# Performance work log

Hardware: AMD Instinct MI355X
Metric: run time of the kernel (lower is better)

Reference implementation:

```python
import jax, jax.numpy as jnp
import numpy as np

DIM = 512
HEADS = 8
DIM_HEAD = 64
INNER = HEADS * DIM_HEAD  # 512
EPS = 1e-5


def _per_head_layernorm(t, gamma, beta):
    # t: [b, h, n, k]; gamma/beta: [h, k] (distinct LayerNorm per head)
    mu = jnp.mean(t, axis=-1, keepdims=True)
    var = jnp.mean(jnp.square(t - mu), axis=-1, keepdims=True)
    t_hat = (t - mu) * jax.lax.rsqrt(var + EPS)
    return t_hat * gamma[None, :, None, :] + beta[None, :, None, :]


def setup_inputs() -> dict:
    key = jax.random.key(0)
    ks = jax.random.split(key, 6)
    x = jax.random.normal(ks[0], (4, 8192, DIM), dtype=jnp.float32)
    # xavier_normal_ with gain=1e-4 on to_qkv weight [3*inner, dim]
    std_qkv = 1e-4 * np.sqrt(2.0 / (3 * INNER + DIM))
    W_qkv = jax.random.normal(ks[1], (3 * INNER, DIM), dtype=jnp.float32) * std_qkv
    gamma_K = jnp.ones((HEADS, DIM_HEAD), dtype=jnp.float32)
    beta_K = jnp.zeros((HEADS, DIM_HEAD), dtype=jnp.float32)
    gamma_V = jnp.ones((HEADS, DIM_HEAD), dtype=jnp.float32)
    beta_V = jnp.zeros((HEADS, DIM_HEAD), dtype=jnp.float32)
    std_out = np.sqrt(1.0 / INNER)
    W_out = jax.random.uniform(ks[2], (DIM, INNER), dtype=jnp.float32, minval=-std_out, maxval=std_out)
    b_out = jax.random.uniform(ks[3], (DIM,), dtype=jnp.float32, minval=-std_out, maxval=std_out)
    return {"x": x, "W_qkv": W_qkv, "gamma_K": gamma_K, "beta_K": beta_K,
            "gamma_V": gamma_V, "beta_V": beta_V, "W_out": W_out, "b_out": b_out}


def reference(x, W_qkv, gamma_K, beta_K, gamma_V, beta_V, W_out, b_out):
    b, n, _ = x.shape
    qkv = jnp.einsum('bnd,ed->bne', x, W_qkv)  # [b, n, 3*inner]
    q, k, v = jnp.split(qkv, 3, axis=-1)

    def to_heads(t):  # [b, n, h*k] -> [b, h, n, k]
        return t.reshape(b, n, HEADS, DIM_HEAD).transpose(0, 2, 1, 3)

    q, k, v = to_heads(q), to_heads(k), to_heads(v)
    k = _per_head_layernorm(k, gamma_K, beta_K)
    v = _per_head_layernorm(v, gamma_V, beta_V)

    # Galerkin linear attention: (K^T V)/n then Q @ (.)  -> O(n * d^2)
    p_attn = jnp.einsum('bhnk,bhnv->bhkv', k, v) / n  # [b, h, k, k]
    out = jnp.einsum('bhnk,bhkv->bhnv', q, p_attn)    # [b, h, n, k]
    out = out.transpose(0, 2, 1, 3).reshape(b, n, INNER)
    return jnp.einsum('bne,de->bnd', out, W_out) + b_out
```

## Files before the change

### kernel.cpp

```cpp
#include <hip/hip_runtime.h>


typedef __attribute__((ext_vector_type(8))) short bf16x8;
typedef __attribute__((ext_vector_type(4))) float f32x4;
typedef __attribute__((ext_vector_type(4))) unsigned short u16x4;
typedef __attribute__((ext_vector_type(4))) unsigned int u32x4;

__device__ __forceinline__ unsigned short f2bf(float f) {
  unsigned int u = __builtin_bit_cast(unsigned int, f);
  u += 0x7FFFu + ((u >> 16) & 1u);
  return (unsigned short)(u >> 16);
}

__device__ __forceinline__ float bf2f(unsigned short h) {
  unsigned int u = ((unsigned int)h) << 16;
  return __builtin_bit_cast(float, u);
}

__device__ __forceinline__ unsigned int cvt2(float lo, float hi) {
  return ((unsigned int)f2bf(hi) << 16) | (unsigned int)f2bf(lo);
}

__device__ __forceinline__ f32x4 mfma16(bf16x8 a, bf16x8 b, f32x4 c) {
  return __builtin_amdgcn_mfma_f32_16x16x32_bf16(a, b, c, 0, 0, 0);
}

__device__ __forceinline__ void gload16(const void* g, void* l) {
  __builtin_amdgcn_global_load_lds(
      (const __attribute__((address_space(1))) void*)g,
      (__attribute__((address_space(3))) void*)l, 16, 0, 0);
}

__global__ void k_cvt_w(const float* __restrict__ Wqkv,
                        const float* __restrict__ Wout,
                        unsigned short* __restrict__ Wb,
                        unsigned short* __restrict__ Wob) {
  int i = blockIdx.x * 256 + threadIdx.x;
  const float4* src;
  u16x4* dst;
  if (i < 196608) { src = (const float4*)Wqkv + i; dst = (u16x4*)Wb + i; }
  else { i -= 196608; src = (const float4*)Wout + i; dst = (u16x4*)Wob + i; }
  float4 v = *src;
  u16x4 o;
  o[0] = f2bf(v.x); o[1] = f2bf(v.y); o[2] = f2bf(v.z); o[3] = f2bf(v.w);
  *dst = o;
}

__launch_bounds__(256, 3)
__global__ void k1_kvp(const float* __restrict__ x,
                       const unsigned short* __restrict__ wqkvb,
                       const float* __restrict__ gK, const float* __restrict__ bK,
                       const float* __restrict__ gV, const float* __restrict__ bV,
                       unsigned short* __restrict__ Ppart) {
  __shared__ __align__(16) unsigned short As[8192];
  __shared__ __align__(16) unsigned short Bs[8192];
  const int bid = (int)blockIdx.x;
  const int wgid = (bid & 7) * 256 + (bid >> 3);
  const int rt = wgid >> 3, h = wgid & 7;
  const int tid = (int)threadIdx.x;
  const int l = tid & 63, w = tid >> 6;
  const int wr = w >> 1, wc = w & 1;
  const int g = l >> 4, c16 = l & 15;
  const int row0 = rt * 128;
  const int swz = ((l & 7) ^ (l >> 3)) * 8;

  const float* gx = x + (size_t)(row0 + w * 32 + (l >> 3)) * 512 + swz;
  const int bcol = (w < 2) ? (512 + h * 64 + w * 32) : (1024 + h * 64 + (w - 2) * 32);
  const unsigned short* gsB = wqkvb + (bcol + (l >> 3)) * 512 + swz;
  unsigned short* la = As + w * 2048 + l * 8;

  f32x4 acc[4][4] = {};
  float4 pf[8];

#pragma unroll
  for (int j = 0; j < 4; ++j) {
    pf[2 * j]     = *(const float4*)(gx + j * 4096);
    pf[2 * j + 1] = *(const float4*)(gx + j * 4096 + 4);
  }

  for (int kt = 0; kt < 8; ++kt) {
#pragma unroll
    for (int j = 0; j < 4; ++j) {
      u32x4 c;
      c[0] = cvt2(pf[2 * j].x, pf[2 * j].y);
      c[1] = cvt2(pf[2 * j].z, pf[2 * j].w);
      c[2] = cvt2(pf[2 * j + 1].x, pf[2 * j + 1].y);
      c[3] = cvt2(pf[2 * j + 1].z, pf[2 * j + 1].w);
      *(u32x4*)(la + j * 512) = c;
    }
#pragma unroll
    for (int j = 0; j < 4; ++j)
      gload16(gsB + kt * 64 + j * 8 * 512, Bs + w * 2048 + j * 512);
    __builtin_amdgcn_sched_barrier(0);
    if (kt < 7) {
#pragma unroll
      for (int j = 0; j < 4; ++j) {
        pf[2 * j]     = *(const float4*)(gx + (kt + 1) * 64 + j * 4096);
        pf[2 * j + 1] = *(const float4*)(gx + (kt + 1) * 64 + j * 4096 + 4);
      }
      asm volatile("s_waitcnt vmcnt(8) lgkmcnt(0)" ::: "memory");
    } else {
      asm volatile("s_waitcnt vmcnt(0) lgkmcnt(0)" ::: "memory");
    }
    __builtin_amdgcn_sched_barrier(0);
    __builtin_amdgcn_s_barrier();
#pragma unroll
    for (int ks = 0; ks < 2; ++ks) {
      const int kcol = (ks * 32 + g * 8) ^ ((c16 & 7) << 3);
      bf16x8 af[4], bfv[4];
#pragma unroll
      for (int mi = 0; mi < 4; ++mi)
        af[mi] = *(const bf16x8*)&As[(wr * 64 + mi * 16 + c16) * 64 + kcol];
#pragma unroll
      for (int ni = 0; ni < 4; ++ni)
        bfv[ni] = *(const bf16x8*)&Bs[(wc * 64 + ni * 16 + c16) * 64 + kcol];
#pragma unroll
      for (int mi = 0; mi < 4; ++mi)
#pragma unroll
        for (int ni = 0; ni < 4; ++ni)
          acc[mi][ni] = mfma16(af[mi], bfv[ni], acc[mi][ni]);
    }
    __builtin_amdgcn_sched_barrier(0);
    __builtin_amdgcn_s_barrier();
  }

  const float* gamma = (wc == 0) ? gK : gV;
  const float* beta  = (wc == 0) ? bK : bV;
  float gm[4], bt[4];
#pragma unroll
  for (int ni = 0; ni < 4; ++ni) {
    gm[ni] = gamma[h * 64 + ni * 16 + c16];
    bt[ni] = beta[h * 64 + ni * 16 + c16];
  }
  unsigned short* dst = (wc == 0) ? As : Bs;
#pragma unroll
  for (int mi = 0; mi < 4; ++mi) {
    float mean4[4], rs4[4];
#pragma unroll
    for (int r = 0; r < 4; ++r) {
      float a0 = acc[mi][0][r], a1 = acc[mi][1][r];
      float a2 = acc[mi][2][r], a3 = acc[mi][3][r];
      float s1 = a0 + a1 + a2 + a3;
      float s2 = a0 * a0 + a1 * a1 + a2 * a2 + a3 * a3;
#pragma unroll
      for (int m = 1; m <= 8; m <<= 1) {
        s1 += __shfl_xor(s1, m, 64);
        s2 += __shfl_xor(s2, m, 64);
      }
      const float mean = s1 * (1.0f / 64.0f);
      const float var = s2 * (1.0f / 64.0f) - mean * mean;
      mean4[r] = mean;
      rs4[r] = rsqrtf(var + 1e-5f);
    }
    const int n0 = wr * 64 + mi * 16 + g * 4;
#pragma unroll
    for (int ni = 0; ni < 4; ++ni) {
      u16x4 o;
#pragma unroll
      for (int r = 0; r < 4; ++r)
        o[r] = f2bf((acc[mi][ni][r] - mean4[r]) * rs4[r] * gm[ni] + bt[ni]);
      *(u16x4*)&dst[(ni * 16 + c16) * 128 + (((n0 >> 3) ^ c16) << 3) + (n0 & 7)] = o;
    }
  }
  __syncthreads();

  f32x4 pacc[4] = {};
#pragma unroll
  for (int ks = 0; ks < 4; ++ks) {
    const int grp = ((ks * 4 + g) ^ c16) << 3;
    bf16x8 af = *(const bf16x8*)&As[(w * 16 + c16) * 128 + grp];
#pragma unroll
    for (int ni = 0; ni < 4; ++ni) {
      bf16x8 bv = *(const bf16x8*)&Bs[(ni * 16 + c16) * 128 + grp];
      pacc[ni] = mfma16(af, bv, pacc[ni]);
    }
  }
  const int bh = (rt >> 6) * 8 + h;
  unsigned short* Pp = Ppart + ((size_t)(bh * 64 + (rt & 63))) * 4096;
#pragma unroll
  for (int ni = 0; ni < 4; ++ni)
#pragma unroll
    for (int r = 0; r < 4; ++r)
      Pp[(w * 16 + g * 4 + r) * 64 + ni * 16 + c16] = f2bf(pacc[ni][r]);
}

__launch_bounds__(256)
__global__ void k_preduce(const unsigned short* __restrict__ Ppart,
                          float* __restrict__ P) {
  const int bh = blockIdx.x;
  const int e = blockIdx.y * 256 + threadIdx.x;
  const unsigned short* src = Ppart + (size_t)bh * 64 * 4096 + e;
  float s = 0.f;
#pragma unroll 8
  for (int sl = 0; sl < 64; ++sl) s += bf2f(src[sl * 4096]);
  P[bh * 4096 + e] = s;
}

__launch_bounds__(256)
__global__ void k3a_g(const float* __restrict__ Wqkv,
                      const float* __restrict__ P,
                      unsigned short* __restrict__ Gt) {
  __shared__ float Pl[64 * 64];
  const int bh = blockIdx.x, dd = blockIdx.y;
  const int b = bh >> 3, h = bh & 7;
  const int t = (int)threadIdx.x;
  for (int i = t; i < 1024; i += 256)
    ((float4*)Pl)[i] = ((const float4*)(P + bh * 4096))[i];
  __syncthreads();

  const int qg = t >> 6, dl = t & 63;
  const int d = dd * 64 + dl;
  float acc[16] = {};
  for (int dh = 0; dh < 64; ++dh) {
    const float wq = Wqkv[(h * 64 + dh) * 512 + d];
    const float* pr = &Pl[dh * 64 + qg * 16];
#pragma unroll
    for (int i = 0; i < 16; ++i) acc[i] += pr[i] * wq;
  }
  unsigned short* go = &Gt[(b * 512 + d) * 512 + h * 64 + qg * 16];
#pragma unroll
  for (int i = 0; i < 16; ++i) go[i] = f2bf(acc[i] * (1.0f / 8192.0f));
}

__device__ __forceinline__ void stage_tile(const unsigned short* pa,
                                           const unsigned short* pb,
                                           unsigned short* As, unsigned short* Bs,
                                           int w) {
#pragma unroll
  for (int j = 0; j < 4; ++j) {
    gload16(pa + j * 8 * 512, As + w * 2048 + j * 512);
    gload16(pb + j * 8 * 512, Bs + w * 2048 + j * 512);
  }
}

__device__ __forceinline__ void compute_tile(const unsigned short* As,
                                             const unsigned short* Bs,
                                             int wr, int wc, int g, int c16,
                                             f32x4 acc[4][4]) {
#pragma unroll
  for (int ks = 0; ks < 2; ++ks) {
    const int kcol = (ks * 32 + g * 8) ^ ((c16 & 7) << 3);
    bf16x8 af[4], bfv[4];
#pragma unroll
    for (int mi = 0; mi < 4; ++mi)
      af[mi] = *(const bf16x8*)&As[(wr * 64 + mi * 16 + c16) * 64 + kcol];
#pragma unroll
    for (int ni = 0; ni < 4; ++ni)
      bfv[ni] = *(const bf16x8*)&Bs[(wc * 64 + ni * 16 + c16) * 64 + kcol];
#pragma unroll
    for (int mi = 0; mi < 4; ++mi)
#pragma unroll
      for (int ni = 0; ni < 4; ++ni)
        acc[mi][ni] = mfma16(af[mi], bfv[ni], acc[mi][ni]);
  }
}

__launch_bounds__(256)
__global__ void k3b_m(const unsigned short* __restrict__ wob,
                      const unsigned short* __restrict__ Gt,
                      unsigned short* __restrict__ Mb) {
  __shared__ __align__(16) unsigned short As[8192];
  __shared__ __align__(16) unsigned short Bs[8192];
  const int rt = blockIdx.x, ct = blockIdx.y, b = blockIdx.z;
  const int tid = (int)threadIdx.x;
  const int l = tid & 63, w = tid >> 6;
  const int wr = w >> 1, wc = w & 1;
  const int g = l >> 4, c16 = l & 15;
  const int row0 = rt * 128, col0 = ct * 128;
  const int swz = ((l & 7) ^ (l >> 3)) * 8;

  const unsigned short* gsA = wob + (row0 + w * 32 + (l >> 3)) * 512 + swz;
  const unsigned short* gsB = Gt + b * 262144 + (col0 + w * 32 + (l >> 3)) * 512 + swz;

  f32x4 acc[4][4] = {};
  for (int kt = 0; kt < 8; ++kt) {
    stage_tile(gsA + kt * 64, gsB + kt * 64, As, Bs, w);
    __syncthreads();
    compute_tile(As, Bs, wr, wc, g, c16, acc);
    __syncthreads();
  }

#pragma unroll
  for (int mi = 0; mi < 4; ++mi)
#pragma unroll
    for (int ni = 0; ni < 4; ++ni) {
      const int colg = col0 + wc * 64 + ni * 16 + c16;
#pragma unroll
      for (int r = 0; r < 4; ++r) {
        const int rowg = row0 + wr * 64 + mi * 16 + g * 4 + r;
        Mb[(b * 512 + rowg) * 512 + colg] = f2bf(acc[mi][ni][r]);
      }
    }
}

__launch_bounds__(256, 3)
__global__ void k4_final(const float* __restrict__ x,
                         const unsigned short* __restrict__ Mb,
                         const float* __restrict__ bout,
                         float* __restrict__ y) {
  __shared__ __align__(16) unsigned short As[8192];
  __shared__ __align__(16) unsigned short Bs[8192];
  const int bid = (int)blockIdx.x;
  const int wgid = (bid & 7) * 128 + (bid >> 3);
  const int rt = wgid >> 2, ct = wgid & 3;
  const int tid = (int)threadIdx.x;
  const int l = tid & 63, w = tid >> 6;
  const int wr = w >> 1, wc = w & 1;
  const int g = l >> 4, c16 = l & 15;
  const int row0 = rt * 128, col0 = ct * 128;
  const int bb = row0 >> 13;
  const int swz = ((l & 7) ^ (l >> 3)) * 8;

  const float* gx = x + (size_t)(row0 + w * 32 + (l >> 3)) * 512 + swz;
  const unsigned short* gsB =
      Mb + (size_t)bb * 262144 + (col0 + w * 32 + (l >> 3)) * 512 + swz;
  unsigned short* la = As + w * 2048 + l * 8;

  f32x4 acc[4][4] = {};
  float4 pf[8];
#pragma unroll
  for (int j = 0; j < 4; ++j) {
    pf[2 * j]     = *(const float4*)(gx + j * 4096);
    pf[2 * j + 1] = *(const float4*)(gx + j * 4096 + 4);
  }

  for (int kt = 0; kt < 8; ++kt) {
#pragma unroll
    for (int j = 0; j < 4; ++j) {
      u32x4 c;
      c[0] = cvt2(pf[2 * j].x, pf[2 * j].y);
      c[1] = cvt2(pf[2 * j].z, pf[2 * j].w);
      c[2] = cvt2(pf[2 * j + 1].x, pf[2 * j + 1].y);
      c[3] = cvt2(pf[2 * j + 1].z, pf[2 * j + 1].w);
      *(u32x4*)(la + j * 512) = c;
    }
#pragma unroll
    for (int j = 0; j < 4; ++j)
      gload16(gsB + kt * 64 + j * 8 * 512, Bs + w * 2048 + j * 512);
    __builtin_amdgcn_sched_barrier(0);
    if (kt < 7) {
#pragma unroll
      for (int j = 0; j < 4; ++j) {
        pf[2 * j]     = *(const float4*)(gx + (kt + 1) * 64 + j * 4096);
        pf[2 * j + 1] = *(const float4*)(gx + (kt + 1) * 64 + j * 4096 + 4);
      }
      asm volatile("s_waitcnt vmcnt(8) lgkmcnt(0)" ::: "memory");
    } else {
      asm volatile("s_waitcnt vmcnt(0) lgkmcnt(0)" ::: "memory");
    }
    __builtin_amdgcn_sched_barrier(0);
    __builtin_amdgcn_s_barrier();
#pragma unroll
    for (int ks = 0; ks < 2; ++ks) {
      const int kcol = (ks * 32 + g * 8) ^ ((c16 & 7) << 3);
      bf16x8 af[4], bfv[4];
#pragma unroll
      for (int mi = 0; mi < 4; ++mi)
        af[mi] = *(const bf16x8*)&As[(wr * 64 + mi * 16 + c16) * 64 + kcol];
#pragma unroll
      for (int ni = 0; ni < 4; ++ni)
        bfv[ni] = *(const bf16x8*)&Bs[(wc * 64 + ni * 16 + c16) * 64 + kcol];
#pragma unroll
      for (int mi = 0; mi < 4; ++mi)
#pragma unroll
        for (int ni = 0; ni < 4; ++ni)
          acc[mi][ni] = mfma16(af[mi], bfv[ni], acc[mi][ni]);
    }
    __builtin_amdgcn_sched_barrier(0);
    __builtin_amdgcn_s_barrier();
  }

  float bo[4];
#pragma unroll
  for (int ni = 0; ni < 4; ++ni)
    bo[ni] = bout[col0 + wc * 64 + ni * 16 + c16];
#pragma unroll
  for (int mi = 0; mi < 4; ++mi)
#pragma unroll
    for (int ni = 0; ni < 4; ++ni) {
      const int colg = col0 + wc * 64 + ni * 16 + c16;
#pragma unroll
      for (int r = 0; r < 4; ++r) {
        const int rowg = row0 + wr * 64 + mi * 16 + g * 4 + r;
        y[rowg * 512 + colg] = acc[mi][ni][r] + bo[ni];
      }
    }
}

extern "C" void kernel_launch(void* const* d_in, const int* in_sizes, int n_in,
                              void* d_out, int out_size, void* d_ws, size_t ws_size,
                              hipStream_t stream) {
  (void)in_sizes; (void)n_in; (void)out_size; (void)ws_size;
  const float* x    = (const float*)d_in[0];
  const float* Wqkv = (const float*)d_in[1];
  const float* gK   = (const float*)d_in[2];
  const float* bK   = (const float*)d_in[3];
  const float* gV   = (const float*)d_in[4];
  const float* bV   = (const float*)d_in[5];
  const float* Wout = (const float*)d_in[6];
  const float* bout = (const float*)d_in[7];
  float* y = (float*)d_out;

  char* w = (char*)d_ws;
  unsigned short* Wb    = (unsigned short*)(w);
  unsigned short* Wob   = (unsigned short*)(w + 1572864);
  float*          P     = (float*)         (w + 2097152);
  unsigned short* Gt    = (unsigned short*)(w + 2621440);
  unsigned short* Mb    = (unsigned short*)(w + 4718592);
  unsigned short* Ppart = (unsigned short*)(w + 6815744);

  k_cvt_w<<<1024, 256, 0, stream>>>(Wqkv, Wout, Wb, Wob);

  k1_kvp<<<2048, 256, 0, stream>>>(x, Wb, gK, bK, gV, bV, Ppart);
  k_preduce<<<dim3(32, 16), 256, 0, stream>>>(Ppart, P);
  k3a_g<<<dim3(32, 8), 256, 0, stream>>>(Wqkv, P, Gt);
  k3b_m<<<dim3(4, 4, 4), 256, 0, stream>>>(Wob, Gt, Mb);
  k4_final<<<1024, 256, 0, stream>>>(x, Mb, bout, y);
}
```

Baseline: 125.6 us.

## Halve k1 row tile to 64 rows with two-wave workgroups

Shrinks the KV projection plus K^T·V kernel from 128-row, 4-wave tiles to 64-row, 2-wave tiles. One wave now computes the full K block and the other the full V block. The launch doubles to 4096 smaller workgroups, and the partial-P buffer and its reduction grow from 64 to 128 slices per batch-head. The aim is more workgroups in flight and less LDS per block. The cost is that the bf16 weight tiles are reloaded twice as often, and the partial-P writes and reduction reads double.

```diff
diff --git a/kernel.cpp b/kernel.cpp
--- a/kernel.cpp
+++ b/kernel.cpp
@@ -46,27 +46,26 @@
   *dst = o;
 }
 
-__launch_bounds__(256, 3)
+__launch_bounds__(128, 4)
 __global__ void k1_kvp(const float* __restrict__ x,
                        const unsigned short* __restrict__ wqkvb,
                        const float* __restrict__ gK, const float* __restrict__ bK,
                        const float* __restrict__ gV, const float* __restrict__ bV,
                        unsigned short* __restrict__ Ppart) {
-  __shared__ __align__(16) unsigned short As[8192];
+  __shared__ __align__(16) unsigned short As[4096];
   __shared__ __align__(16) unsigned short Bs[8192];
   const int bid = (int)blockIdx.x;
-  const int wgid = (bid & 7) * 256 + (bid >> 3);
+  const int wgid = (bid & 7) * 512 + (bid >> 3);
   const int rt = wgid >> 3, h = wgid & 7;
   const int tid = (int)threadIdx.x;
   const int l = tid & 63, w = tid >> 6;
-  const int wr = w >> 1, wc = w & 1;
   const int g = l >> 4, c16 = l & 15;
-  const int row0 = rt * 128;
+  const int row0 = rt * 64;
   const int swz = ((l & 7) ^ (l >> 3)) * 8;
 
   const float* gx = x + (size_t)(row0 + w * 32 + (l >> 3)) * 512 + swz;
-  const int bcol = (w < 2) ? (512 + h * 64 + w * 32) : (1024 + h * 64 + (w - 2) * 32);
-  const unsigned short* gsB = wqkvb + (bcol + (l >> 3)) * 512 + swz;
+  const int bbase = (w == 0) ? 512 : 1024;
+  const unsigned short* gsB = wqkvb + (bbase + h * 64 + (l >> 3)) * 512 + swz;
   unsigned short* la = As + w * 2048 + l * 8;
 
   f32x4 acc[4][4] = {};
@@ -89,8 +88,8 @@
       *(u32x4*)(la + j * 512) = c;
     }
 #pragma unroll
-    for (int j = 0; j < 4; ++j)
-      gload16(gsB + kt * 64 + j * 8 * 512, Bs + w * 2048 + j * 512);
+    for (int j = 0; j < 8; ++j)
+      gload16(gsB + kt * 64 + j * 8 * 512, Bs + w * 4096 + j * 512);
     __builtin_amdgcn_sched_barrier(0);
     if (kt < 7) {
 #pragma unroll
@@ -110,10 +109,10 @@
       bf16x8 af[4], bfv[4];
 #pragma unroll
       for (int mi = 0; mi < 4; ++mi)
-        af[mi] = *(const bf16x8*)&As[(wr * 64 + mi * 16 + c16) * 64 + kcol];
+        af[mi] = *(const bf16x8*)&As[(mi * 16 + c16) * 64 + kcol];
 #pragma unroll
       for (int ni = 0; ni < 4; ++ni)
-        bfv[ni] = *(const bf16x8*)&Bs[(wc * 64 + ni * 16 + c16) * 64 + kcol];
+        bfv[ni] = *(const bf16x8*)&Bs[w * 4096 + (ni * 16 + c16) * 64 + kcol];
 #pragma unroll
       for (int mi = 0; mi < 4; ++mi)
 #pragma unroll
@@ -124,15 +123,15 @@
     __builtin_amdgcn_s_barrier();
   }
 
-  const float* gamma = (wc == 0) ? gK : gV;
-  const float* beta  = (wc == 0) ? bK : bV;
+  const float* gamma = (w == 0) ? gK : gV;
+  const float* beta  = (w == 0) ? bK : bV;
   float gm[4], bt[4];
 #pragma unroll
   for (int ni = 0; ni < 4; ++ni) {
     gm[ni] = gamma[h * 64 + ni * 16 + c16];
     bt[ni] = beta[h * 64 + ni * 16 + c16];
   }
-  unsigned short* dst = (wc == 0) ? As : Bs;
+  unsigned short* dst = (w == 0) ? As : Bs;
 #pragma unroll
   for (int mi = 0; mi < 4; ++mi) {
     float mean4[4], rs4[4];
@@ -152,36 +151,47 @@
       mean4[r] = mean;
       rs4[r] = rsqrtf(var + 1e-5f);
     }
-    const int n0 = wr * 64 + mi * 16 + g * 4;
+    const int n0 = mi * 16 + g * 4;
 #pragma unroll
     for (int ni = 0; ni < 4; ++ni) {
       u16x4 o;
 #pragma unroll
       for (int r = 0; r < 4; ++r)
         o[r] = f2bf((acc[mi][ni][r] - mean4[r]) * rs4[r] * gm[ni] + bt[ni]);
-      *(u16x4*)&dst[(ni * 16 + c16) * 128 + (((n0 >> 3) ^ c16) << 3) + (n0 & 7)] = o;
+      *(u16x4*)&dst[(ni * 16 + c16) * 64 + (((n0 >> 3) ^ (c16 & 7)) << 3) + (n0 & 7)] = o;
     }
   }
   __syncthreads();
 
-  f32x4 pacc[4] = {};
-#pragma unroll
-  for (int ks = 0; ks < 4; ++ks) {
-    const int grp = ((ks * 4 + g) ^ c16) << 3;
-    bf16x8 af = *(const bf16x8*)&As[(w * 16 + c16) * 128 + grp];
-#pragma unroll
-    for (int ni = 0; ni < 4; ++ni) {
-      bf16x8 bv = *(const bf16x8*)&Bs[(ni * 16 + c16) * 128 + grp];
-      pacc[ni] = mfma16(af, bv, pacc[ni]);
-    }
-  }
-  const int bh = (rt >> 6) * 8 + h;
-  unsigned short* Pp = Ppart + ((size_t)(bh * 64 + (rt & 63))) * 4096;
-#pragma unroll
-  for (int ni = 0; ni < 4; ++ni)
-#pragma unroll
-    for (int r = 0; r < 4; ++r)
-      Pp[(w * 16 + g * 4 + r) * 64 + ni * 16 + c16] = f2bf(pacc[ni][r]);
+  const unsigned short* Kl = As;
+  const unsigned short* Vl = Bs;
+  f32x4 pacc[2][4] = {};
+#pragma unroll
+  for (int ks = 0; ks < 2; ++ks) {
+    const int grp = (((ks * 4 + g) ^ (c16 & 7)) << 3);
+    bf16x8 af[2], bv[4];
+#pragma unroll
+    for (int m2 = 0; m2 < 2; ++m2)
+      af[m2] = *(const bf16x8*)&Kl[(w * 32 + m2 * 16 + c16) * 64 + grp];
+#pragma unroll
+    for (int ni = 0; ni < 4; ++ni)
+      bv[ni] = *(const bf16x8*)&Vl[(ni * 16 + c16) * 64 + grp];
+#pragma unroll
+    for (int m2 = 0; m2 < 2; ++m2)
+#pragma unroll
+      for (int ni = 0; ni < 4; ++ni)
+        pacc[m2][ni] = mfma16(af[m2], bv[ni], pacc[m2][ni]);
+  }
+  const int bh = (rt >> 7) * 8 + h;
+  unsigned short* Pp = Ppart + ((size_t)(bh * 128 + (rt & 127))) * 4096;
+#pragma unroll
+  for (int m2 = 0; m2 < 2; ++m2)
+#pragma unroll
+    for (int ni = 0; ni < 4; ++ni)
+#pragma unroll
+      for (int r = 0; r < 4; ++r)
+        Pp[(w * 32 + m2 * 16 + g * 4 + r) * 64 + ni * 16 + c16] =
+            f2bf(pacc[m2][ni][r]);
 }
 
 __launch_bounds__(256)
@@ -189,10 +199,10 @@
                           float* __restrict__ P) {
   const int bh = blockIdx.x;
   const int e = blockIdx.y * 256 + threadIdx.x;
-  const unsigned short* src = Ppart + (size_t)bh * 64 * 4096 + e;
+  const unsigned short* src = Ppart + (size_t)bh * 128 * 4096 + e;
   float s = 0.f;
 #pragma unroll 8
-  for (int sl = 0; sl < 64; ++sl) s += bf2f(src[sl * 4096]);
+  for (int sl = 0; sl < 128; ++sl) s += bf2f(src[sl * 4096]);
   P[bh * 4096 + e] = s;
 }
 
@@ -411,7 +421,7 @@
 
   k_cvt_w<<<1024, 256, 0, stream>>>(Wqkv, Wout, Wb, Wob);
 
-  k1_kvp<<<2048, 256, 0, stream>>>(x, Wb, gK, bK, gV, bV, Ppart);
+  k1_kvp<<<4096, 128, 0, stream>>>(x, Wb, gK, bK, gV, bV, Ppart);
   k_preduce<<<dim3(32, 16), 256, 0, stream>>>(Ppart, P);
   k3a_g<<<dim3(32, 8), 256, 0, stream>>>(Wqkv, P, Gt);
   k3b_m<<<dim3(4, 4, 4), 256, 0, stream>>>(Wob, Gt, Mb);
```

Result: slower. 151.5 us (+20.6%).
